# Kernel tuning notes

Measured on AMD Instinct MI355X. Metric: run time of the kernel, lower is better.

The kernel has to match this reference:

```python
import jax, jax.numpy as jnp
import numpy as np

EMBED_DIM = 256
UNITS = 512


def setup_inputs() -> dict:
    key = jax.random.key(0)
    ks = jax.random.split(key, 8)
    B, L = 2048, 64  # batch, 8*8 spatial locations
    features = jax.random.normal(ks[0], (B, L, EMBED_DIM), dtype=jnp.float32)
    hidden = jax.random.normal(ks[1], (B, UNITS), dtype=jnp.float32)
    s1 = 1.0 / np.sqrt(EMBED_DIM)
    s2 = 1.0 / np.sqrt(UNITS)
    W1 = jax.random.normal(ks[2], (EMBED_DIM, UNITS), dtype=jnp.float32) * s1
    b1 = jnp.zeros((UNITS,), dtype=jnp.float32)
    W2 = jax.random.normal(ks[3], (UNITS, UNITS), dtype=jnp.float32) * s2
    b2 = jnp.zeros((UNITS,), dtype=jnp.float32)
    V = jax.random.normal(ks[4], (UNITS, 1), dtype=jnp.float32) * s2
    bv = jnp.zeros((1,), dtype=jnp.float32)
    return {"features": features, "hidden": hidden, "W1": W1, "b1": b1,
            "W2": W2, "b2": b2, "V": V, "bv": bv}


def reference(features, hidden, W1, b1, W2, b2, V, bv):
    # features: [B, L, E], hidden: [B, U]
    # Bahdanau additive attention
    proj_f = jnp.einsum('ble,eu->blu', features, W1) + b1          # [B, L, U]
    proj_h = (hidden @ W2 + b2)[:, None, :]                        # [B, 1, U]
    e = jnp.tanh(proj_f + proj_h)                                  # [B, L, U]
    score = jnp.einsum('blu,uo->blo', e, V) + bv                   # [B, L, 1]
    attention_weights = jax.nn.softmax(score, axis=1)              # [B, L, 1]
    context_vector = jnp.sum(attention_weights * features, axis=1) # [B, E]
    return context_vector, attention_weights
```

## Files before the change

kernel.cpp:

```cpp
#include <hip/hip_runtime.h>
#include <math.h>

#define BATCH 2048
#define LDIM 64
#define EDIM 256
#define UDIM 512

typedef __attribute__((ext_vector_type(8))) _Float16 half8;
typedef __attribute__((ext_vector_type(4))) _Float16 half4;
typedef __attribute__((ext_vector_type(4))) float floatx4;

__device__ inline float tanh_fast(float x) {
    float t = __builtin_amdgcn_exp2f(x * 2.88539008177792681f);
    return 1.f - 2.f * __builtin_amdgcn_rcpf(t + 1.f);
}
__device__ inline half8 cvt8(float4 f0, float4 f1) {
    half8 h;
    h[0] = (_Float16)f0.x; h[1] = (_Float16)f0.y;
    h[2] = (_Float16)f0.z; h[3] = (_Float16)f0.w;
    h[4] = (_Float16)f1.x; h[5] = (_Float16)f1.y;
    h[6] = (_Float16)f1.z; h[7] = (_Float16)f1.w;
    return h;
}
__device__ inline half4 cvt4(float4 f) {
    half4 h;
    h[0] = (_Float16)f.x; h[1] = (_Float16)f.y;
    h[2] = (_Float16)f.z; h[3] = (_Float16)f.w;
    return h;
}
__device__ inline const half8* bfrag(const unsigned short* F, int kc, int ntg, int l) {
    return (const half8*)(F + ((((size_t)kc * 32 + ntg) * 64 + l) << 3));
}

__global__ __launch_bounds__(256) void prep_frag(const float* __restrict__ W1,
                                                 const float* __restrict__ W2,
                                                 unsigned short* __restrict__ F1,
                                                 unsigned short* __restrict__ F2) {
    __shared__ float S[32 * 128];
    int bid = blockIdx.x;
    const float* W; unsigned short* F; int kc, grp;
    if (bid < 32) { W = W1; F = F1; kc = bid >> 2; grp = bid & 3; }
    else { bid -= 32; W = W2; F = F2; kc = bid >> 2; grp = bid & 3; }
    const int tid = threadIdx.x;
    const float* src = W + (size_t)kc * 32 * UDIM + grp * 128;
    float4* Sv = (float4*)S;
#pragma unroll
    for (int i = 0; i < 4; ++i) {
        int f = tid + i * 256;
        int k = f >> 5, c4 = f & 31;
        Sv[f] = *(const float4*)(src + (size_t)k * UDIM + c4 * 4);
    }
    __syncthreads();
#pragma unroll
    for (int i = 0; i < 2; ++i) {
        int u = tid + i * 256;
        int lane = u & 63, ntl = u >> 6;
        int n_loc = ntl * 16 + (lane & 15);
        int k0 = (lane >> 4) * 8;
        half8 h;
#pragma unroll
        for (int j = 0; j < 8; ++j)
            h[j] = (_Float16)S[(k0 + j) * 128 + n_loc];
        int ntg = grp * 8 + ntl;
        *(half8*)(F + (((size_t)kc * 32 + ntg) * 64 + lane) * 8) = h;
    }
}

__global__ __launch_bounds__(256) void prep_ph(const float* __restrict__ hidden,
                                               const unsigned short* __restrict__ F2,
                                               const float* __restrict__ b1,
                                               const float* __restrict__ b2,
                                               float* __restrict__ ph) {
    const int tid = threadIdx.x;
    const int w = tid >> 6;
    const int l = tid & 63;
    const int r0 = blockIdx.x * 16;

    floatx4 acc[8];
#pragma unroll
    for (int i = 0; i < 8; ++i) acc[i] = (floatx4){0.f, 0.f, 0.f, 0.f};

    const float* ap = hidden + (size_t)(r0 + (l & 15)) * UDIM + ((l >> 4) << 3);

    float4 a0 = *(const float4*)(ap);
    float4 a1 = *(const float4*)(ap + 4);
    half8 B[8];
#pragma unroll
    for (int nt = 0; nt < 8; ++nt) B[nt] = *bfrag(F2, 0, w * 8 + nt, l);

    for (int kc = 0; kc < 16; ++kc) {
        half8 a = cvt8(a0, a1);
        float4 n0, n1; half8 NB[8];
        if (kc < 15) {
            n0 = *(const float4*)(ap + (kc + 1) * 32);
            n1 = *(const float4*)(ap + (kc + 1) * 32 + 4);
#pragma unroll
            for (int nt = 0; nt < 8; ++nt) NB[nt] = *bfrag(F2, kc + 1, w * 8 + nt, l);
        }
#pragma unroll
        for (int nt = 0; nt < 8; ++nt)
            acc[nt] = __builtin_amdgcn_mfma_f32_16x16x32_f16(a, B[nt], acc[nt], 0, 0, 0);
        if (kc < 15) {
            a0 = n0; a1 = n1;
#pragma unroll
            for (int nt = 0; nt < 8; ++nt) B[nt] = NB[nt];
        }
    }
#pragma unroll
    for (int nt = 0; nt < 8; ++nt) {
        const int n = (w * 8 + nt) * 16 + (l & 15);
        const float bias = b1[n] + b2[n];
#pragma unroll
        for (int r = 0; r < 4; ++r) {
            const int m = (l >> 4) * 4 + r;
            ph[(size_t)(r0 + m) * UDIM + n] = acc[nt][r] + bias;
        }
    }
}

__global__ __launch_bounds__(512, 4) void attn_main(
    const float* __restrict__ feat, const unsigned short* __restrict__ F1,
    const float* __restrict__ ph, const float* __restrict__ Vw,
    const float* __restrict__ bv,
    float* __restrict__ ctx_out, float* __restrict__ w_out)
{
    __shared__ _Float16 lS[2][4][64][8];
    __shared__ float phl[512];
    __shared__ float Vl[512];
    __shared__ float scp[8][64];
    __shared__ float wsm[64];
    __shared__ float ctxp[2][256];

    const int tid = threadIdx.x;
    const int w = tid >> 6;
    const int l = tid & 63;
    const size_t b = blockIdx.x;
    const float* fb = feat + b * (LDIM * EDIM);

    const int r  = tid >> 3, q = tid & 7;
    const int mt_s = r >> 4;
    const int fl   = (q >> 1) * 16 + (r & 15);
    const int h4   = (q & 1) * 4;

    {
        float4 g = *(const float4*)(fb + r * EDIM + q * 4);
        phl[tid] = ph[b * UDIM + tid];
        Vl[tid]  = Vw[tid];
        *(half4*)&lS[0][mt_s][fl ^ 0][h4] = cvt4(g);
    }
    __syncthreads();

    floatx4 acc[4][4];
#pragma unroll
    for (int i = 0; i < 4; ++i)
#pragma unroll
        for (int j = 0; j < 4; ++j) acc[i][j] = (floatx4){0.f, 0.f, 0.f, 0.f};

    for (int kc = 0; kc < 8; ++kc) {
        float4 g;
        if (kc < 7)
            g = *(const float4*)(fb + r * EDIM + (kc + 1) * 32 + q * 4);

        half8 Bc[4];
#pragma unroll
        for (int nt = 0; nt < 4; ++nt) Bc[nt] = *bfrag(F1, kc, w * 4 + nt, l);
#pragma unroll
        for (int mt = 0; mt < 4; ++mt) {
            const half8 a = *(const half8*)&lS[kc & 1][mt][l ^ kc][0];
#pragma unroll
            for (int nt = 0; nt < 4; ++nt)
                acc[nt][mt] = __builtin_amdgcn_mfma_f32_16x16x32_f16(
                    a, Bc[nt], acc[nt][mt], 0, 0, 0);
        }

        if (kc < 7) {
            *(half4*)&lS[(kc + 1) & 1][mt_s][fl ^ (kc + 1)][h4] = cvt4(g);
            __syncthreads();
        }
    }

    float sv[4][4];
#pragma unroll
    for (int mt = 0; mt < 4; ++mt)
#pragma unroll
        for (int rr = 0; rr < 4; ++rr) sv[mt][rr] = 0.f;
#pragma unroll
    for (int nt = 0; nt < 4; ++nt) {
        const int n = (w * 4 + nt) * 16 + (l & 15);
        const float phn = phl[n];
        const float vn  = Vl[n];
#pragma unroll
        for (int mt = 0; mt < 4; ++mt)
#pragma unroll
            for (int rr = 0; rr < 4; ++rr)
                sv[mt][rr] += tanh_fast(acc[nt][mt][rr] + phn) * vn;
    }
#pragma unroll
    for (int mt = 0; mt < 4; ++mt)
#pragma unroll
        for (int rr = 0; rr < 4; ++rr) {
            float v = sv[mt][rr];
            v += __shfl_xor(v, 1);
            v += __shfl_xor(v, 2);
            v += __shfl_xor(v, 4);
            v += __shfl_xor(v, 8);
            if ((l & 15) == 0) scp[w][mt * 16 + (l >> 4) * 4 + rr] = v;
        }
    __syncthreads();

    if (tid < 64) {
        float s = bv[0];
#pragma unroll
        for (int wv = 0; wv < 8; ++wv) s += scp[wv][tid];
        float m = s;
        m = fmaxf(m, __shfl_xor(m, 32));
        m = fmaxf(m, __shfl_xor(m, 16));
        m = fmaxf(m, __shfl_xor(m, 8));
        m = fmaxf(m, __shfl_xor(m, 4));
        m = fmaxf(m, __shfl_xor(m, 2));
        m = fmaxf(m, __shfl_xor(m, 1));
        float e = __builtin_amdgcn_exp2f((s - m) * 1.44269504088896341f);
        float sum = e;
        sum += __shfl_xor(sum, 32);
        sum += __shfl_xor(sum, 16);
        sum += __shfl_xor(sum, 8);
        sum += __shfl_xor(sum, 4);
        sum += __shfl_xor(sum, 2);
        sum += __shfl_xor(sum, 1);
        float wgt = e / sum;
        wsm[tid] = wgt;
        w_out[b * LDIM + tid] = wgt;
    }
    __syncthreads();

    {
        const int e = tid & 255, h = tid >> 8;
        float c = 0.f;
#pragma unroll 8
        for (int ll = h * 32; ll < h * 32 + 32; ++ll)
            c = fmaf(wsm[ll], fb[ll * EDIM + e], c);
        ctxp[h][e] = c;
    }
    __syncthreads();
    if (tid < 256)
        ctx_out[b * EDIM + tid] = ctxp[0][tid] + ctxp[1][tid];
}

extern "C" void kernel_launch(void* const* d_in, const int* in_sizes, int n_in,
                              void* d_out, int out_size, void* d_ws, size_t ws_size,
                              hipStream_t stream) {
    const float* features = (const float*)d_in[0];
    const float* hidden   = (const float*)d_in[1];
    const float* W1       = (const float*)d_in[2];
    const float* b1       = (const float*)d_in[3];
    const float* W2       = (const float*)d_in[4];
    const float* b2       = (const float*)d_in[5];
    const float* Vw       = (const float*)d_in[6];
    const float* bv       = (const float*)d_in[7];

    float* ctx_out = (float*)d_out;
    float* w_out   = (float*)d_out + (size_t)BATCH * EDIM;

    float* ph = (float*)d_ws;
    unsigned short* F1 = (unsigned short*)(ph + (size_t)BATCH * UDIM);
    unsigned short* F2 = F1 + (size_t)8 * 32 * 64 * 8;

    prep_frag<<<dim3(96), dim3(256), 0, stream>>>(W1, W2, F1, F2);
    prep_ph<<<dim3(128), dim3(256), 0, stream>>>(hidden, F2, b1, b2, ph);
    attn_main<<<dim3(BATCH), dim3(512), 0, stream>>>(
        features, F1, ph, Vw, bv, ctx_out, w_out);
}
```

Before: 255.3 us.

## Merge weight-fragment prep and hidden projection into one prep kernel

Result: slower. 272.5 us (+6.7%).

```diff
diff --git a/kernel.cpp b/kernel.cpp
--- a/kernel.cpp
+++ b/kernel.cpp
@@ -32,83 +32,88 @@
     return (const half8*)(F + ((((size_t)kc * 32 + ntg) * 64 + l) << 3));
 }
 
-__global__ __launch_bounds__(256) void prep_frag(const float* __restrict__ W1,
-                                                 const float* __restrict__ W2,
-                                                 unsigned short* __restrict__ F1,
-                                                 unsigned short* __restrict__ F2) {
-    __shared__ float S[32 * 128];
-    int bid = blockIdx.x;
-    const float* W; unsigned short* F; int kc, grp;
-    if (bid < 32) { W = W1; F = F1; kc = bid >> 2; grp = bid & 3; }
-    else { bid -= 32; W = W2; F = F2; kc = bid >> 2; grp = bid & 3; }
+__global__ __launch_bounds__(512) void prep_all(
+    const float* __restrict__ W1, const float* __restrict__ W2,
+    const float* __restrict__ hidden,
+    const float* __restrict__ b1, const float* __restrict__ b2,
+    unsigned short* __restrict__ F1, float* __restrict__ ph)
+{
+    __shared__ float S[32 * 512];
     const int tid = threadIdx.x;
-    const float* src = W + (size_t)kc * 32 * UDIM + grp * 128;
-    float4* Sv = (float4*)S;
-#pragma unroll
-    for (int i = 0; i < 4; ++i) {
-        int f = tid + i * 256;
-        int k = f >> 5, c4 = f & 31;
-        Sv[f] = *(const float4*)(src + (size_t)k * UDIM + c4 * 4);
-    }
-    __syncthreads();
-#pragma unroll
-    for (int i = 0; i < 2; ++i) {
-        int u = tid + i * 256;
-        int lane = u & 63, ntl = u >> 6;
-        int n_loc = ntl * 16 + (lane & 15);
-        int k0 = (lane >> 4) * 8;
-        half8 h;
-#pragma unroll
-        for (int j = 0; j < 8; ++j)
-            h[j] = (_Float16)S[(k0 + j) * 128 + n_loc];
-        int ntg = grp * 8 + ntl;
-        *(half8*)(F + (((size_t)kc * 32 + ntg) * 64 + lane) * 8) = h;
-    }
-}
-
-__global__ __launch_bounds__(256) void prep_ph(const float* __restrict__ hidden,
-                                               const unsigned short* __restrict__ F2,
-                                               const float* __restrict__ b1,
-                                               const float* __restrict__ b2,
-                                               float* __restrict__ ph) {
-    const int tid = threadIdx.x;
+    const int bid = blockIdx.x;
+
+    if (bid < 16) {
+        const int half = tid >> 8;
+        const int t    = tid & 255;
+        const int u    = bid * 2 + half;
+        const int kc   = u >> 2, grp = u & 3;
+        float* Sh = S + half * (32 * 128);
+        const float* src = W1 + (size_t)kc * 32 * UDIM + grp * 128;
+        float4* Sv = (float4*)Sh;
+#pragma unroll
+        for (int i = 0; i < 4; ++i) {
+            int f = t + i * 256;
+            int k = f >> 5, c4 = f & 31;
+            Sv[f] = *(const float4*)(src + (size_t)k * UDIM + c4 * 4);
+        }
+        __syncthreads();
+#pragma unroll
+        for (int i = 0; i < 2; ++i) {
+            int uu = t + i * 256;
+            int lane = uu & 63, ntl = uu >> 6;
+            int n_loc = ntl * 16 + (lane & 15);
+            int k0 = (lane >> 4) * 8;
+            half8 h;
+#pragma unroll
+            for (int j = 0; j < 8; ++j)
+                h[j] = (_Float16)Sh[(k0 + j) * 128 + n_loc];
+            int ntg = grp * 8 + ntl;
+            *(half8*)(F1 + (((size_t)kc * 32 + ntg) * 64 + lane) * 8) = h;
+        }
+        return;
+    }
+
+    const int bp = bid - 16;
+    const int r0 = bp * 16;
     const int w = tid >> 6;
     const int l = tid & 63;
-    const int r0 = blockIdx.x * 16;
-
-    floatx4 acc[8];
-#pragma unroll
-    for (int i = 0; i < 8; ++i) acc[i] = (floatx4){0.f, 0.f, 0.f, 0.f};
+    const int k0 = (l >> 4) * 8;
+
+    floatx4 acc[4];
+#pragma unroll
+    for (int i = 0; i < 4; ++i) acc[i] = (floatx4){0.f, 0.f, 0.f, 0.f};
 
     const float* ap = hidden + (size_t)(r0 + (l & 15)) * UDIM + ((l >> 4) << 3);
 
-    float4 a0 = *(const float4*)(ap);
-    float4 a1 = *(const float4*)(ap + 4);
-    half8 B[8];
-#pragma unroll
-    for (int nt = 0; nt < 8; ++nt) B[nt] = *bfrag(F2, 0, w * 8 + nt, l);
-
     for (int kc = 0; kc < 16; ++kc) {
+#pragma unroll
+        for (int i = 0; i < 8; ++i) {
+            int unit = tid + 512 * i;
+            int row = unit >> 7, c4 = unit & 127;
+            *(float4*)&S[row * 512 + c4 * 4] =
+                *(const float4*)(W2 + ((size_t)(kc * 32 + row)) * UDIM + c4 * 4);
+        }
+        __syncthreads();
+
+        float4 a0 = *(const float4*)(ap + kc * 32);
+        float4 a1 = *(const float4*)(ap + kc * 32 + 4);
         half8 a = cvt8(a0, a1);
-        float4 n0, n1; half8 NB[8];
-        if (kc < 15) {
-            n0 = *(const float4*)(ap + (kc + 1) * 32);
-            n1 = *(const float4*)(ap + (kc + 1) * 32 + 4);
-#pragma unroll
-            for (int nt = 0; nt < 8; ++nt) NB[nt] = *bfrag(F2, kc + 1, w * 8 + nt, l);
-        }
-#pragma unroll
-        for (int nt = 0; nt < 8; ++nt)
-            acc[nt] = __builtin_amdgcn_mfma_f32_16x16x32_f16(a, B[nt], acc[nt], 0, 0, 0);
-        if (kc < 15) {
-            a0 = n0; a1 = n1;
-#pragma unroll
-            for (int nt = 0; nt < 8; ++nt) B[nt] = NB[nt];
-        }
-    }
-#pragma unroll
-    for (int nt = 0; nt < 8; ++nt) {
-        const int n = (w * 8 + nt) * 16 + (l & 15);
+
+#pragma unroll
+        for (int nt = 0; nt < 4; ++nt) {
+            const int ncol = (w * 4 + nt) * 16 + (l & 15);
+            half8 bf;
+#pragma unroll
+            for (int j = 0; j < 8; ++j)
+                bf[j] = (_Float16)S[(k0 + j) * 512 + ncol];
+            acc[nt] = __builtin_amdgcn_mfma_f32_16x16x32_f16(a, bf, acc[nt], 0, 0, 0);
+        }
+        __syncthreads();
+    }
+
+#pragma unroll
+    for (int nt = 0; nt < 4; ++nt) {
+        const int n = (w * 4 + nt) * 16 + (l & 15);
         const float bias = b1[n] + b2[n];
 #pragma unroll
         for (int r = 0; r < 4; ++r) {
@@ -263,10 +268,8 @@
 
     float* ph = (float*)d_ws;
     unsigned short* F1 = (unsigned short*)(ph + (size_t)BATCH * UDIM);
-    unsigned short* F2 = F1 + (size_t)8 * 32 * 64 * 8;
-
-    prep_frag<<<dim3(96), dim3(256), 0, stream>>>(W1, W2, F1, F2);
-    prep_ph<<<dim3(128), dim3(256), 0, stream>>>(hidden, F2, b1, b2, ph);
+
+    prep_all<<<dim3(144), dim3(512), 0, stream>>>(W1, W2, hidden, b1, b2, F1, ph);
     attn_main<<<dim3(BATCH), dim3(512), 0, stream>>>(
         features, F1, ph, Vw, bv, ctx_out, w_out);
 }
```
